# Performance work log

Hardware: AMD Instinct MI355X
Metric: run time of the kernel (lower is better)

Reference implementation:

```python
import jax, jax.numpy as jnp
import numpy as np

# config (matches init_kwargs)
NA, NEN = 8, 8            # n_agents, n_enemies
NENT = NA + NEN           # n_entities
NFA, NFE = 64, 64         # state_nf_al, state_nf_en
E, A, M, HE = 64, 64, 32, 64  # entity_embed, attn_embed, mixing_embed, hypernet_embed
TD, TE = 64, 64           # task_repre_dim, task_repre_embed_dim
BS, SL = 64, 512


def setup_inputs() -> dict:
    key = jax.random.key(0)
    ks = iter(jax.random.split(key, 32))
    def rn(shape, scale=0.05):
        return jax.random.normal(next(ks), shape, dtype=jnp.float32) * scale
    return {
        "agent_qs": rn((BS, SL, NA), 1.0),
        "states": rn((BS, SL, NA * NFA + NEN * NFE), 1.0),
        "task_repre_mu": rn((BS, SL, NA, TD), 1.0),
        "ally_w": rn((NFA, E)), "ally_b": rn((E,)),
        "enemy_w": rn((NFE, E)), "enemy_b": rn((E,)),
        "q_w": rn((E, A)), "q_b": rn((A,)),
        "k_w": rn((E, A)), "k_b": rn((A,)),
        "hw1_w1": rn((E + NFA + TE, HE)), "hw1_b1": rn((HE,)),
        "hw1_w2": rn((HE, M)), "hw1_b2": rn((M,)),
        "hwf_w1": rn((E + TE, HE)), "hwf_b1": rn((HE,)),
        "hwf_w2": rn((HE, M)), "hwf_b2": rn((M,)),
        "hb1_w": rn((E + TE, M)), "hb1_b": rn((M,)),
        "v_w1": rn((E + TE, M)), "v_b1": rn((M,)),
        "v_w2": rn((M, 1)), "v_b2": rn((1,)),
        "tre_w": rn((TD, TE)), "tre_b": rn((TE,)),
    }


def reference(agent_qs, states, task_repre_mu,
              ally_w, ally_b, enemy_w, enemy_b,
              q_w, q_b, k_w, k_b,
              hw1_w1, hw1_b1, hw1_w2, hw1_b2,
              hwf_w1, hwf_b1, hwf_w2, hwf_b2,
              hb1_w, hb1_b, v_w1, v_b1, v_w2, v_b2,
              tre_w, tre_b):
    bs, sl = agent_qs.shape[:2]
    # decompose_state (state_last_action=False, state_timestep_number=False)
    ally = states[..., : NA * NFA].reshape(bs, sl, NA, NFA)      # [bs,sl,NA,NFA]
    enemy = states[..., NA * NFA:].reshape(bs, sl, NEN, NFE)     # [bs,sl,NEN,NFE]
    ally_e = ally @ ally_w + ally_b                              # [bs,sl,NA,E]
    enemy_e = enemy @ enemy_w + enemy_b                          # [bs,sl,NEN,E]
    ent = jnp.concatenate([ally_e, enemy_e], axis=2)             # [bs,sl,NENT,E]
    q = ent @ q_w + q_b                                          # [bs,sl,NENT,A]
    k = ent @ k_w + k_b
    energy = jnp.einsum('bsqa,bska->bsqk', q, k)                 # [bs,sl,NENT,NENT]
    # torch: F.softmax(energy, dim=1) on [B,n_ent,n_ent] -> softmax over query axis
    attn = jax.nn.softmax(energy, axis=2)
    # attn_out = bmm(value[B,E,n], attn[B,n,n]).mean(-1)
    attn_out = jnp.einsum('bsne,bsnk->bse', ent, attn) / NENT    # [bs,sl,E]

    mean_mu = task_repre_mu.mean(axis=-2)                        # [bs,sl,TD]
    tre = task_repre_mu @ tre_w + tre_b                          # [bs,sl,NA,TE]
    mean_tre = mean_mu @ tre_w + tre_b                           # [bs,sl,TE]

    ent_mix = jnp.concatenate([
        jnp.broadcast_to(attn_out[:, :, None, :], (bs, sl, NA, E)),
        ally, tre], axis=-1)                                     # [bs,sl,NA,E+NFA+TE]
    mix = jnp.concatenate([attn_out, mean_tre], axis=-1)         # [bs,sl,E+TE]

    w1 = jnp.abs(jax.nn.relu(ent_mix @ hw1_w1 + hw1_b1) @ hw1_w2 + hw1_b2)  # [bs,sl,NA,M]
    b1 = mix @ hb1_w + hb1_b                                     # [bs,sl,M]
    hidden = jax.nn.elu(jnp.einsum('bsn,bsnm->bsm', agent_qs, w1) + b1)     # [bs,sl,M]
    wf = jnp.abs(jax.nn.relu(mix @ hwf_w1 + hwf_b1) @ hwf_w2 + hwf_b2)      # [bs,sl,M]
    v = jax.nn.relu(mix @ v_w1 + v_b1) @ v_w2 + v_b2             # [bs,sl,1]
    q_tot = jnp.einsum('bsm,bsm->bs', hidden, wf)[..., None] + v # [bs,sl,1]
    return q_tot
```

## Files before the change

### kernel.cpp

```cpp
#include <hip/hip_runtime.h>
#include <math.h>


#define TOKS 32768

typedef __attribute__((ext_vector_type(8))) short short8;
typedef __attribute__((ext_vector_type(4))) float f32x4;

#define MFMA(a, b, c) __builtin_amdgcn_mfma_f32_16x16x32_bf16((a), (b), (c), 0, 0, 0)

#define E_CAT   0
#define E_WQKT  8192
#define E_ZBRT  13312
#define E_H1T   29696
#define E_W2T   41984
#define E_WFT   44032
#define E_BF16_TOTAL 46080
#define E_AO_US 46464

__device__ __forceinline__ unsigned short bfr(float x) {
    unsigned u = __builtin_bit_cast(unsigned, x);
    u += 0x7fffu + ((u >> 16) & 1u);
    return (unsigned short)(u >> 16);
}
__device__ __forceinline__ float bf2f(unsigned short h) {
    unsigned u = ((unsigned)h) << 16;
    return __builtin_bit_cast(float, u);
}
__device__ __forceinline__ short8 cvt8v(float4 a, float4 b) {
    short8 r;
    r[0] = (short)bfr(a.x); r[1] = (short)bfr(a.y);
    r[2] = (short)bfr(a.z); r[3] = (short)bfr(a.w);
    r[4] = (short)bfr(b.x); r[5] = (short)bfr(b.y);
    r[6] = (short)bfr(b.z); r[7] = (short)bfr(b.w);
    return r;
}
#define SWZ64(r, c)  ((((r) * 64)  + (c)) ^ (((r) & 7) << 3))
#define SWZ128(r, c) ((((r) * 128) + (c)) ^ (((r) & 7) << 3))
#define SWZ192(r, c) ((((r) * 192) + (c)) ^ (((r) & 7) << 3))

__global__ __launch_bounds__(256) void qmix_setup(
    const float* __restrict__ ally_w, const float* __restrict__ enemy_w,
    const float* __restrict__ q_w, const float* __restrict__ k_w,
    const float* __restrict__ k_b,
    const float* __restrict__ hw1_w1, const float* __restrict__ hw1_b1,
    const float* __restrict__ hw1_w2,
    const float* __restrict__ hwf_w1, const float* __restrict__ hwf_b1,
    const float* __restrict__ hwf_w2,
    const float* __restrict__ hb1_w, const float* __restrict__ hb1_b,
    const float* __restrict__ v_w1, const float* __restrict__ v_b1,
    const float* __restrict__ tre_w, const float* __restrict__ tre_b,
    unsigned short* __restrict__ wsb, float* __restrict__ wsf)
{
    int gid = blockIdx.x * 256 + threadIdx.x;
    if (gid < E_BF16_TOTAL) {
        float v = 0.f;
        int base, r, c, K;
        if (gid < E_WQKT) {
            base = E_CAT; K = 128;
            int i = gid - base; r = i >> 7; c = i & 127;
            v = (c < 64) ? ally_w[c * 64 + r] : enemy_w[(c - 64) * 64 + r];
        } else if (gid < E_ZBRT) {
            base = E_WQKT; K = 64;
            int i = gid - base; r = i >> 6; c = i & 63;
            if (r < 64) {
                for (int g = 0; g < 64; ++g) v += q_w[c * 64 + g] * k_w[r * 64 + g];
            } else if (r == 64) {
                for (int g = 0; g < 64; ++g) v += q_w[c * 64 + g] * k_b[g];
            }
        } else if (gid < E_H1T) {
            base = E_ZBRT; K = 128;
            int i = gid - base; r = i >> 7; c = i & 127;
            if (r < 64) {
                if (c < 64) v = hwf_w1[c * 64 + r];
                else for (int g = 0; g < 64; ++g) v += tre_w[(c - 64) * 64 + g] * hwf_w1[(64 + g) * 64 + r];
            } else if (r < 96) {
                int m = r - 64;
                if (c < 64) v = hb1_w[c * 32 + m];
                else for (int g = 0; g < 64; ++g) v += tre_w[(c - 64) * 64 + g] * hb1_w[(64 + g) * 32 + m];
            } else {
                int m = r - 96;
                if (c < 64) v = v_w1[c * 32 + m];
                else for (int g = 0; g < 64; ++g) v += tre_w[(c - 64) * 64 + g] * v_w1[(64 + g) * 32 + m];
            }
        } else if (gid < E_W2T) {
            base = E_H1T; K = 192;
            int i = gid - base; r = i / 192; c = i % 192;
            if (c < 64) v = hw1_w1[(64 + c) * 64 + r];
            else if (c < 128) {
                for (int g = 0; g < 64; ++g) v += tre_w[(c - 64) * 64 + g] * hw1_w1[(128 + g) * 64 + r];
            } else v = hw1_w1[(c - 128) * 64 + r];
        } else if (gid < E_WFT) {
            base = E_W2T; K = 64;
            int i = gid - base; r = i >> 6; c = i & 63;
            v = hw1_w2[c * 32 + r];
        } else {
            base = E_WFT; K = 64;
            int i = gid - base; r = i >> 6; c = i & 63;
            v = hwf_w2[c * 32 + r];
        }
        wsb[base + ((r * K + c) ^ ((r & 7) << 3))] = bfr(v);
    } else if (gid < E_BF16_TOTAL + 192) {
        int j = gid - E_BF16_TOTAL; float v;
        if (j < 64) {
            v = hw1_b1[j];
            for (int g = 0; g < 64; ++g) v += tre_b[g] * hw1_w1[(128 + g) * 64 + j];
        } else if (j < 128) {
            int e = j - 64; v = hwf_b1[e];
            for (int g = 0; g < 64; ++g) v += tre_b[g] * hwf_w1[(64 + g) * 64 + e];
        } else if (j < 160) {
            int m = j - 128; v = hb1_b[m];
            for (int g = 0; g < 64; ++g) v += tre_b[g] * hb1_w[(64 + g) * 32 + m];
        } else {
            int m = j - 160; v = v_b1[m];
            for (int g = 0; g < 64; ++g) v += tre_b[g] * v_w1[(64 + g) * 32 + m];
        }
        wsf[j] = v;
    }
}

__global__ __launch_bounds__(512) void qmix_attn(
    const float* __restrict__ states,
    const float* __restrict__ ally_b, const float* __restrict__ enemy_b,
    const unsigned short* __restrict__ wsb,
    unsigned short* __restrict__ aoG)
{
    __shared__ unsigned short sWa[13312];
    __shared__ unsigned short sE[8][1024];
    __shared__ unsigned short sT[8][1024];

    const int lane = threadIdx.x & 63;
    const int wv   = threadIdx.x >> 6;
    const int l15  = lane & 15;
    const int lg   = lane >> 4;
    const int kb   = lg * 8;
    const size_t t = (size_t)blockIdx.x * 8 + wv;

    const short8 zero8 = {0, 0, 0, 0, 0, 0, 0, 0};
    const f32x4  zero4 = {0.f, 0.f, 0.f, 0.f};

    for (int i = threadIdx.x * 8; i < 13312; i += 512 * 8)
        *(short8*)(sWa + i) = *(const short8*)(wsb + E_CAT + i);

    const int roff = (l15 < 8) ? (l15 * 64 + kb) : (512 + (l15 - 8) * 64 + kb);
    const float* p = states + t * 1024 + roff;
    float4 cur0 = *(const float4*)(p);
    float4 cur1 = *(const float4*)(p + 4);
    float4 cur2 = *(const float4*)(p + 32);
    float4 cur3 = *(const float4*)(p + 36);

    float biasEnt[4];
    #pragma unroll
    for (int nt = 0; nt < 4; ++nt) {
        int col = nt * 16 + l15;
        biasEnt[nt] = (lg < 2) ? ally_b[col] : enemy_b[col];
    }
    __syncthreads();
    const unsigned short* lCAT  = sWa;
    const unsigned short* lWQKT = sWa + 8192;

    unsigned short* E = sE[wv];
    unsigned short* T = sT[wv];

    short8 a01 = cvt8v(cur0, cur1);
    short8 a23 = cvt8v(cur2, cur3);
    const bool isally = (l15 < 8);

    f32x4 accB[4] = {zero4, zero4, zero4, zero4};
    #pragma unroll
    for (int ks = 0; ks < 4; ++ks) {
        short8 af;
        if (ks == 0)      af = isally ? a01 : zero8;
        else if (ks == 1) af = isally ? a23 : zero8;
        else if (ks == 2) af = isally ? zero8 : a01;
        else              af = isally ? zero8 : a23;
        #pragma unroll
        for (int nt = 0; nt < 4; ++nt) {
            short8 w = *(const short8*)&lCAT[SWZ128(nt * 16 + l15, ks * 32 + kb)];
            accB[nt] = MFMA(af, w, accB[nt]);
        }
    }
    float entv[4][4];
    #pragma unroll
    for (int nt = 0; nt < 4; ++nt) {
        #pragma unroll
        for (int reg = 0; reg < 4; ++reg) {
            entv[nt][reg] = accB[nt][reg] + biasEnt[nt];
            E[SWZ64(lg * 4 + reg, nt * 16 + l15)] = bfr(entv[nt][reg]);
        }
    }

    f32x4 accC[5] = {zero4, zero4, zero4, zero4, zero4};
    short8 ef0 = *(const short8*)&E[SWZ64(l15, 0 * 32 + kb)];
    short8 ef1 = *(const short8*)&E[SWZ64(l15, 1 * 32 + kb)];
    #pragma unroll
    for (int nt = 0; nt < 5; ++nt) {
        short8 w0 = *(const short8*)&lWQKT[SWZ64(nt * 16 + l15, 0 * 32 + kb)];
        short8 w1 = *(const short8*)&lWQKT[SWZ64(nt * 16 + l15, 1 * 32 + kb)];
        accC[nt] = MFMA(ef0, w0, accC[nt]);
        accC[nt] = MFMA(ef1, w1, accC[nt]);
    }
    const int src = lane & 48;
    float si[4];
    #pragma unroll
    for (int reg = 0; reg < 4; ++reg) si[reg] = __shfl(accC[4][reg], src);
    #pragma unroll
    for (int nt = 0; nt < 4; ++nt)
        #pragma unroll
        for (int reg = 0; reg < 4; ++reg)
            T[SWZ64(lg * 4 + reg, nt * 16 + l15)] = bfr(accC[nt][reg]);

    f32x4 en = zero4;
    {
        short8 ta0 = *(const short8*)&T[SWZ64(l15, 0 * 32 + kb)];
        short8 ta1 = *(const short8*)&T[SWZ64(l15, 1 * 32 + kb)];
        en = MFMA(ta0, ef0, en);
        en = MFMA(ta1, ef1, en);
    }
    #pragma unroll
    for (int reg = 0; reg < 4; ++reg) en[reg] += si[reg];

    float mx = fmaxf(fmaxf(en[0], en[1]), fmaxf(en[2], en[3]));
    mx = fmaxf(mx, __shfl_xor(mx, 16));
    mx = fmaxf(mx, __shfl_xor(mx, 32));
    float p0 = __expf(en[0] - mx), p1 = __expf(en[1] - mx);
    float p2 = __expf(en[2] - mx), p3 = __expf(en[3] - mx);
    float s = p0 + p1 + p2 + p3;
    s += __shfl_xor(s, 16);
    s += __shfl_xor(s, 32);
    float inv = 1.f / s;
    float r0 = p0 * inv, r1 = p1 * inv, r2 = p2 * inv, r3 = p3 * inv;
    r0 += __shfl_xor(r0, 1); r0 += __shfl_xor(r0, 2); r0 += __shfl_xor(r0, 4); r0 += __shfl_xor(r0, 8);
    r1 += __shfl_xor(r1, 1); r1 += __shfl_xor(r1, 2); r1 += __shfl_xor(r1, 4); r1 += __shfl_xor(r1, 8);
    r2 += __shfl_xor(r2, 1); r2 += __shfl_xor(r2, 2); r2 += __shfl_xor(r2, 4); r2 += __shfl_xor(r2, 8);
    r3 += __shfl_xor(r3, 1); r3 += __shfl_xor(r3, 2); r3 += __shfl_xor(r3, 4); r3 += __shfl_xor(r3, 8);

    float part[4];
    #pragma unroll
    for (int nt = 0; nt < 4; ++nt) {
        float pp = r0 * entv[nt][0] + r1 * entv[nt][1]
                 + r2 * entv[nt][2] + r3 * entv[nt][3];
        pp += __shfl_xor(pp, 16);
        pp += __shfl_xor(pp, 32);
        part[nt] = pp;
    }
    float ao = (lg == 0) ? part[0] : (lg == 1) ? part[1]
             : (lg == 2) ? part[2] : part[3];
    aoG[t * 64 + lane] = bfr(ao * 0.0625f);
}

__global__ __launch_bounds__(512) void qmix_hyper(
    const float* __restrict__ agent_qs, const float* __restrict__ states,
    const float* __restrict__ mu,
    const float* __restrict__ v_w2, const float* __restrict__ v_b2,
    const float* __restrict__ hw1_b2, const float* __restrict__ hwf_b2,
    const unsigned short* __restrict__ wsb, const float* __restrict__ wsf,
    const unsigned short* __restrict__ aoG,
    float* __restrict__ out)
{
    __shared__ unsigned short sWb[16384];
    __shared__ unsigned short sMM[8192];
    __shared__ unsigned short sZT[8][1024];
    __shared__ float sB1[8][256];
    __shared__ float sWF[8][256];
    __shared__ float sV[8][8];

    const int tid  = threadIdx.x;
    const int lane = tid & 63;
    const int wv   = tid >> 6;
    const int l15  = lane & 15;
    const int lg   = lane >> 4;
    const int kb   = lg * 8;
    const int T0   = blockIdx.x * 64 + wv * 8;
    const int tokB = blockIdx.x * 64;

    const float* BH1 = wsf + 0;
    const float* BHF = wsf + 64;
    const float* BB1 = wsf + 128;
    const float* BV  = wsf + 160;

    const short8 zero8 = {0, 0, 0, 0, 0, 0, 0, 0};
    const f32x4  zero4 = {0.f, 0.f, 0.f, 0.f};

    for (int i = tid * 8; i < 16384; i += 512 * 8)
        *(short8*)(sWb + i) = *(const short8*)(wsb + E_ZBRT + i);

    {
        const size_t row = (size_t)(T0 + (l15 & 7));
    }
    short8 zA0 = *(const short8*)&aoG[(size_t)(T0 + (l15 & 7)) * 64 + kb];
    short8 zA1 = *(const short8*)&aoG[(size_t)(T0 + (l15 & 7)) * 64 + 32 + kb];

    {
        int tok = tid >> 3;
        int e8  = (tid & 7) * 8;
        const float* mp = mu + (size_t)(tokB + tok) * 512 + e8;
        float s0 = 0.f, s1 = 0.f, s2 = 0.f, s3 = 0.f,
              s4 = 0.f, s5 = 0.f, s6 = 0.f, s7 = 0.f;
        #pragma unroll
        for (int a = 0; a < 8; ++a) {
            float4 u = *(const float4*)(mp + a * 64);
            float4 v = *(const float4*)(mp + a * 64 + 4);
            s0 += u.x; s1 += u.y; s2 += u.z; s3 += u.w;
            s4 += v.x; s5 += v.y; s6 += v.z; s7 += v.w;
        }
        short8 r;
        r[0] = (short)bfr(s0 * 0.125f); r[1] = (short)bfr(s1 * 0.125f);
        r[2] = (short)bfr(s2 * 0.125f); r[3] = (short)bfr(s3 * 0.125f);
        r[4] = (short)bfr(s4 * 0.125f); r[5] = (short)bfr(s5 * 0.125f);
        r[6] = (short)bfr(s6 * 0.125f); r[7] = (short)bfr(s7 * 0.125f);
        *(short8*)&sMM[SWZ64(tok, e8)] = r;
    }
    for (int i = lane; i < 512; i += 64) sZT[wv][512 + i] = 0;
    __syncthreads();

    f32x4 zb[8] = {zero4, zero4, zero4, zero4, zero4, zero4, zero4, zero4};
    const bool arow = (l15 < 8);
    #pragma unroll
    for (int ks = 0; ks < 4; ++ks) {
        short8 af;
        if (ks == 0)      af = arow ? zA0 : zero8;
        else if (ks == 1) af = arow ? zA1 : zero8;
        else {
            short8 m = *(const short8*)&sMM[SWZ64(wv * 8 + (l15 & 7), (ks - 2) * 32 + kb)];
            af = arow ? m : zero8;
        }
        #pragma unroll
        for (int nt = 0; nt < 8; ++nt) {
            short8 w = *(const short8*)&sWb[SWZ128(nt * 16 + l15, ks * 32 + kb)];
            zb[nt] = MFMA(af, w, zb[nt]);
        }
    }
    __syncthreads();

    for (int i = tid * 8; i < 16384; i += 512 * 8)
        *(short8*)(sWb + i) = *(const short8*)(wsb + E_H1T + i);

    if (lg < 2) {
        #pragma unroll
        for (int nt = 0; nt < 4; ++nt) {
            int col = nt * 16 + l15;
            float bz = BHF[col];
            #pragma unroll
            for (int reg = 0; reg < 4; ++reg)
                sZT[wv][SWZ64(lg * 4 + reg, col)] = bfr(fmaxf(zb[nt][reg] + bz, 0.f));
        }
        #pragma unroll
        for (int nt = 4; nt < 6; ++nt) {
            int m = (nt - 4) * 16 + l15;
            float bb = BB1[m];
            #pragma unroll
            for (int reg = 0; reg < 4; ++reg)
                sB1[wv][(lg * 4 + reg) * 32 + m] = zb[nt][reg] + bb;
        }
    }
    {
        float bv0 = BV[l15], bv1 = BV[16 + l15];
        float vw0 = v_w2[l15], vw1 = v_w2[16 + l15];
        #pragma unroll
        for (int reg = 0; reg < 4; ++reg) {
            float vp = fmaxf(zb[6][reg] + bv0, 0.f) * vw0
                     + fmaxf(zb[7][reg] + bv1, 0.f) * vw1;
            vp += __shfl_xor(vp, 1); vp += __shfl_xor(vp, 2);
            vp += __shfl_xor(vp, 4); vp += __shfl_xor(vp, 8);
            if (l15 == 0 && lg < 2) sV[wv][lg * 4 + reg] = vp;
        }
    }
    __syncthreads();
    const unsigned short* lH1T = sWb;
    const unsigned short* lW2T = sWb + 12288;
    const unsigned short* lWFT = sWb + 14336;

    {
        f32x4 wfa = zero4, wfb = zero4;
        #pragma unroll
        for (int ks = 0; ks < 2; ++ks) {
            short8 af = *(const short8*)&sZT[wv][SWZ64(l15, ks * 32 + kb)];
            short8 b0 = *(const short8*)&lWFT[SWZ64(l15, ks * 32 + kb)];
            short8 b1 = *(const short8*)&lWFT[SWZ64(16 + l15, ks * 32 + kb)];
            wfa = MFMA(af, b0, wfa);
            wfb = MFMA(af, b1, wfb);
        }
        if (lg < 2) {
            float hb0 = hwf_b2[l15], hb1 = hwf_b2[16 + l15];
            #pragma unroll
            for (int reg = 0; reg < 4; ++reg) {
                int tok = lg * 4 + reg;
                sWF[wv][tok * 32 + l15]      = fabsf(wfa[reg] + hb0);
                sWF[wv][tok * 32 + 16 + l15] = fabsf(wfb[reg] + hb1);
            }
        }
    }

    const float vb2 = v_b2[0];
    const float b20 = hw1_b2[l15], b21 = hw1_b2[16 + l15];
    const int agent = l15 & 7;
    const int toff  = l15 >> 3;
    unsigned short* tile = sZT[wv];

    float4 cs0, cs1, cs2, cs3, cm0, cm1, cm2, cm3;
    short8 ca0, ca1;
    {
        const size_t tokA = (size_t)(T0 + toff);
        const float* sp = states + tokA * 1024 + agent * 64 + kb;
        const float* mp = mu + tokA * 512 + agent * 64 + kb;
        cs0 = *(const float4*)sp;        cs1 = *(const float4*)(sp + 4);
        cs2 = *(const float4*)(sp + 32); cs3 = *(const float4*)(sp + 36);
        cm0 = *(const float4*)mp;        cm1 = *(const float4*)(mp + 4);
        cm2 = *(const float4*)(mp + 32); cm3 = *(const float4*)(mp + 36);
        ca0 = *(const short8*)&aoG[tokA * 64 + kb];
        ca1 = *(const short8*)&aoG[tokA * 64 + 32 + kb];
    }

    for (int mc = 0; mc < 4; ++mc) {
        float4 us0 = cs0, us1 = cs1, us2 = cs2, us3 = cs3;
        float4 um0 = cm0, um1 = cm1, um2 = cm2, um3 = cm3;
        short8 ua0 = ca0, ua1 = ca1;
        if (mc < 3) {
            const size_t tokA = (size_t)(T0 + (mc + 1) * 2 + toff);
            const float* sp = states + tokA * 1024 + agent * 64 + kb;
            const float* mp = mu + tokA * 512 + agent * 64 + kb;
            cs0 = *(const float4*)sp;        cs1 = *(const float4*)(sp + 4);
            cs2 = *(const float4*)(sp + 32); cs3 = *(const float4*)(sp + 36);
            cm0 = *(const float4*)mp;        cm1 = *(const float4*)(mp + 4);
            cm2 = *(const float4*)(mp + 32); cm3 = *(const float4*)(mp + 36);
            ca0 = *(const short8*)&aoG[tokA * 64 + kb];
            ca1 = *(const short8*)&aoG[tokA * 64 + 32 + kb];
        }
        short8 f0 = cvt8v(us0, us1), f1 = cvt8v(us2, us3);
        short8 f2 = cvt8v(um0, um1), f3 = cvt8v(um2, um3);

        f32x4 h[4] = {zero4, zero4, zero4, zero4};
        #pragma unroll
        for (int ks = 0; ks < 6; ++ks) {
            short8 af = (ks == 0) ? f0 : (ks == 1) ? f1 : (ks == 2) ? f2
                      : (ks == 3) ? f3 : (ks == 4) ? ua0 : ua1;
            #pragma unroll
            for (int nt = 0; nt < 4; ++nt) {
                short8 w = *(const short8*)&lH1T[SWZ192(nt * 16 + l15, ks * 32 + kb)];
                h[nt] = MFMA(af, w, h[nt]);
            }
        }
        #pragma unroll
        for (int nt = 0; nt < 4; ++nt) {
            int col = nt * 16 + l15;
            float bh = BH1[col];
            #pragma unroll
            for (int reg = 0; reg < 4; ++reg)
                tile[SWZ64(lg * 4 + reg, col)] = bfr(fmaxf(h[nt][reg] + bh, 0.f));
        }

        f32x4 wa = zero4, wb = zero4;
        #pragma unroll
        for (int ks = 0; ks < 2; ++ks) {
            short8 af = *(const short8*)&tile[SWZ64(l15, ks * 32 + kb)];
            short8 b0 = *(const short8*)&lW2T[SWZ64(l15, ks * 32 + kb)];
            short8 b1 = *(const short8*)&lW2T[SWZ64(16 + l15, ks * 32 + kb)];
            wa = MFMA(af, b0, wa);
            wb = MFMA(af, b1, wb);
        }

        float hp0 = 0.f, hp1 = 0.f;
        #pragma unroll
        for (int reg = 0; reg < 4; ++reg) {
            int row = lg * 4 + reg;
            float qsv = agent_qs[(size_t)(T0 + mc * 2 + (row >> 3)) * 8 + (row & 7)];
            hp0 += qsv * fabsf(wa[reg] + b20);
            hp1 += qsv * fabsf(wb[reg] + b21);
        }
        hp0 += __shfl_xor(hp0, 16);
        hp1 += __shfl_xor(hp1, 16);
        int tokL = mc * 2 + (lg >> 1);
        float e0 = hp0 + sB1[wv][tokL * 32 + l15];
        float e1 = hp1 + sB1[wv][tokL * 32 + 16 + l15];
        float hid0 = e0 > 0.f ? e0 : (__expf(e0) - 1.f);
        float hid1 = e1 > 0.f ? e1 : (__expf(e1) - 1.f);
        float q = hid0 * sWF[wv][tokL * 32 + l15]
                + hid1 * sWF[wv][tokL * 32 + 16 + l15];
        q += __shfl_xor(q, 1); q += __shfl_xor(q, 2);
        q += __shfl_xor(q, 4); q += __shfl_xor(q, 8);
        if (l15 == 0 && (lg & 1) == 0)
            out[T0 + tokL] = q + sV[wv][tokL] + vb2;
    }
}

extern "C" void kernel_launch(void* const* d_in, const int* in_sizes, int n_in,
                              void* d_out, int out_size, void* d_ws, size_t ws_size,
                              hipStream_t stream)
{
    const float* agent_qs = (const float*)d_in[0];
    const float* states   = (const float*)d_in[1];
    const float* mu       = (const float*)d_in[2];
    const float* ally_w   = (const float*)d_in[3];
    const float* ally_b   = (const float*)d_in[4];
    const float* enemy_w  = (const float*)d_in[5];
    const float* enemy_b  = (const float*)d_in[6];
    const float* q_w      = (const float*)d_in[7];
    const float* k_w      = (const float*)d_in[9];
    const float* k_b      = (const float*)d_in[10];
    const float* hw1_w1   = (const float*)d_in[11];
    const float* hw1_b1   = (const float*)d_in[12];
    const float* hw1_w2   = (const float*)d_in[13];
    const float* hw1_b2   = (const float*)d_in[14];
    const float* hwf_w1   = (const float*)d_in[15];
    const float* hwf_b1   = (const float*)d_in[16];
    const float* hwf_w2   = (const float*)d_in[17];
    const float* hwf_b2   = (const float*)d_in[18];
    const float* hb1_w    = (const float*)d_in[19];
    const float* hb1_b    = (const float*)d_in[20];
    const float* v_w1     = (const float*)d_in[21];
    const float* v_b1     = (const float*)d_in[22];
    const float* v_w2     = (const float*)d_in[23];
    const float* v_b2     = (const float*)d_in[24];
    const float* tre_w    = (const float*)d_in[25];
    const float* tre_b    = (const float*)d_in[26];

    unsigned short* wsb = (unsigned short*)d_ws;
    float* wsf = (float*)((char*)d_ws + (size_t)E_BF16_TOTAL * 2);
    unsigned short* aoG = wsb + E_AO_US;
    float* out = (float*)d_out;

    hipLaunchKernelGGL(qmix_setup, dim3(181), dim3(256), 0, stream,
                       ally_w, enemy_w, q_w, k_w, k_b,
                       hw1_w1, hw1_b1, hw1_w2,
                       hwf_w1, hwf_b1, hwf_w2,
                       hb1_w, hb1_b, v_w1, v_b1, tre_w, tre_b,
                       wsb, wsf);

    hipLaunchKernelGGL(qmix_attn, dim3(TOKS / 8), dim3(512), 0, stream,
                       states, ally_b, enemy_b, wsb, aoG);

    hipLaunchKernelGGL(qmix_hyper, dim3(TOKS / 64), dim3(512), 0, stream,
                       agent_qs, states, mu, v_w2, v_b2, hw1_b2, hwf_b2,
                       wsb, wsf, aoG, out);
}
```

Measured before the change: 88.72 us.

## Fuse attention and hypernet kernels into one per-64-token kernel

Merges the attention kernel into the hypernetwork kernel so each wave computes attention outputs for its 8 tokens in a loop and keeps them in shared memory, removing the global round trip of attention outputs and one kernel launch. Shared memory is reorganized and reused (weights buffer shared across stages, b1 and wf stored as bf16 in per-wave tiles), and the task-mean computation moves into registers per lane. The trade-off is far fewer blocks for the attention phase (512 instead of 4096), so less parallelism and latency hiding for that stage, plus slight extra bf16 rounding of b1 and wf.

```diff
diff --git a/kernel.cpp b/kernel.cpp
--- a/kernel.cpp
+++ b/kernel.cpp
@@ -16,7 +16,6 @@
 #define E_W2T   41984
 #define E_WFT   44032
 #define E_BF16_TOTAL 46080
-#define E_AO_US 46464
 
 __device__ __forceinline__ unsigned short bfr(float x) {
     unsigned u = __builtin_bit_cast(unsigned, x);
@@ -119,150 +118,32 @@
     }
 }
 
-__global__ __launch_bounds__(512) void qmix_attn(
-    const float* __restrict__ states,
-    const float* __restrict__ ally_b, const float* __restrict__ enemy_b,
-    const unsigned short* __restrict__ wsb,
-    unsigned short* __restrict__ aoG)
-{
-    __shared__ unsigned short sWa[13312];
-    __shared__ unsigned short sE[8][1024];
-    __shared__ unsigned short sT[8][1024];
-
-    const int lane = threadIdx.x & 63;
-    const int wv   = threadIdx.x >> 6;
-    const int l15  = lane & 15;
-    const int lg   = lane >> 4;
-    const int kb   = lg * 8;
-    const size_t t = (size_t)blockIdx.x * 8 + wv;
-
-    const short8 zero8 = {0, 0, 0, 0, 0, 0, 0, 0};
-    const f32x4  zero4 = {0.f, 0.f, 0.f, 0.f};
-
-    for (int i = threadIdx.x * 8; i < 13312; i += 512 * 8)
-        *(short8*)(sWa + i) = *(const short8*)(wsb + E_CAT + i);
-
-    const int roff = (l15 < 8) ? (l15 * 64 + kb) : (512 + (l15 - 8) * 64 + kb);
-    const float* p = states + t * 1024 + roff;
-    float4 cur0 = *(const float4*)(p);
-    float4 cur1 = *(const float4*)(p + 4);
-    float4 cur2 = *(const float4*)(p + 32);
-    float4 cur3 = *(const float4*)(p + 36);
-
-    float biasEnt[4];
+__device__ __forceinline__ short8 mmfrag(const float* __restrict__ mp) {
+    float a0 = 0.f, a1 = 0.f, a2 = 0.f, a3 = 0.f, a4 = 0.f, a5 = 0.f, a6 = 0.f, a7 = 0.f;
     #pragma unroll
-    for (int nt = 0; nt < 4; ++nt) {
-        int col = nt * 16 + l15;
-        biasEnt[nt] = (lg < 2) ? ally_b[col] : enemy_b[col];
-    }
-    __syncthreads();
-    const unsigned short* lCAT  = sWa;
-    const unsigned short* lWQKT = sWa + 8192;
-
-    unsigned short* E = sE[wv];
-    unsigned short* T = sT[wv];
-
-    short8 a01 = cvt8v(cur0, cur1);
-    short8 a23 = cvt8v(cur2, cur3);
-    const bool isally = (l15 < 8);
-
-    f32x4 accB[4] = {zero4, zero4, zero4, zero4};
-    #pragma unroll
-    for (int ks = 0; ks < 4; ++ks) {
-        short8 af;
-        if (ks == 0)      af = isally ? a01 : zero8;
-        else if (ks == 1) af = isally ? a23 : zero8;
-        else if (ks == 2) af = isally ? zero8 : a01;
-        else              af = isally ? zero8 : a23;
-        #pragma unroll
-        for (int nt = 0; nt < 4; ++nt) {
-            short8 w = *(const short8*)&lCAT[SWZ128(nt * 16 + l15, ks * 32 + kb)];
-            accB[nt] = MFMA(af, w, accB[nt]);
-        }
-    }
-    float entv[4][4];
-    #pragma unroll
-    for (int nt = 0; nt < 4; ++nt) {
-        #pragma unroll
-        for (int reg = 0; reg < 4; ++reg) {
-            entv[nt][reg] = accB[nt][reg] + biasEnt[nt];
-            E[SWZ64(lg * 4 + reg, nt * 16 + l15)] = bfr(entv[nt][reg]);
-        }
-    }
-
-    f32x4 accC[5] = {zero4, zero4, zero4, zero4, zero4};
-    short8 ef0 = *(const short8*)&E[SWZ64(l15, 0 * 32 + kb)];
-    short8 ef1 = *(const short8*)&E[SWZ64(l15, 1 * 32 + kb)];
-    #pragma unroll
-    for (int nt = 0; nt < 5; ++nt) {
-        short8 w0 = *(const short8*)&lWQKT[SWZ64(nt * 16 + l15, 0 * 32 + kb)];
-        short8 w1 = *(const short8*)&lWQKT[SWZ64(nt * 16 + l15, 1 * 32 + kb)];
-        accC[nt] = MFMA(ef0, w0, accC[nt]);
-        accC[nt] = MFMA(ef1, w1, accC[nt]);
-    }
-    const int src = lane & 48;
-    float si[4];
-    #pragma unroll
-    for (int reg = 0; reg < 4; ++reg) si[reg] = __shfl(accC[4][reg], src);
-    #pragma unroll
-    for (int nt = 0; nt < 4; ++nt)
-        #pragma unroll
-        for (int reg = 0; reg < 4; ++reg)
-            T[SWZ64(lg * 4 + reg, nt * 16 + l15)] = bfr(accC[nt][reg]);
-
-    f32x4 en = zero4;
-    {
-        short8 ta0 = *(const short8*)&T[SWZ64(l15, 0 * 32 + kb)];
-        short8 ta1 = *(const short8*)&T[SWZ64(l15, 1 * 32 + kb)];
-        en = MFMA(ta0, ef0, en);
-        en = MFMA(ta1, ef1, en);
-    }
-    #pragma unroll
-    for (int reg = 0; reg < 4; ++reg) en[reg] += si[reg];
-
-    float mx = fmaxf(fmaxf(en[0], en[1]), fmaxf(en[2], en[3]));
-    mx = fmaxf(mx, __shfl_xor(mx, 16));
-    mx = fmaxf(mx, __shfl_xor(mx, 32));
-    float p0 = __expf(en[0] - mx), p1 = __expf(en[1] - mx);
-    float p2 = __expf(en[2] - mx), p3 = __expf(en[3] - mx);
-    float s = p0 + p1 + p2 + p3;
-    s += __shfl_xor(s, 16);
-    s += __shfl_xor(s, 32);
-    float inv = 1.f / s;
-    float r0 = p0 * inv, r1 = p1 * inv, r2 = p2 * inv, r3 = p3 * inv;
-    r0 += __shfl_xor(r0, 1); r0 += __shfl_xor(r0, 2); r0 += __shfl_xor(r0, 4); r0 += __shfl_xor(r0, 8);
-    r1 += __shfl_xor(r1, 1); r1 += __shfl_xor(r1, 2); r1 += __shfl_xor(r1, 4); r1 += __shfl_xor(r1, 8);
-    r2 += __shfl_xor(r2, 1); r2 += __shfl_xor(r2, 2); r2 += __shfl_xor(r2, 4); r2 += __shfl_xor(r2, 8);
-    r3 += __shfl_xor(r3, 1); r3 += __shfl_xor(r3, 2); r3 += __shfl_xor(r3, 4); r3 += __shfl_xor(r3, 8);
-
-    float part[4];
-    #pragma unroll
-    for (int nt = 0; nt < 4; ++nt) {
-        float pp = r0 * entv[nt][0] + r1 * entv[nt][1]
-                 + r2 * entv[nt][2] + r3 * entv[nt][3];
-        pp += __shfl_xor(pp, 16);
-        pp += __shfl_xor(pp, 32);
-        part[nt] = pp;
-    }
-    float ao = (lg == 0) ? part[0] : (lg == 1) ? part[1]
-             : (lg == 2) ? part[2] : part[3];
-    aoG[t * 64 + lane] = bfr(ao * 0.0625f);
-}
-
-__global__ __launch_bounds__(512) void qmix_hyper(
+    for (int a = 0; a < 8; ++a) {
+        float4 u = *(const float4*)(mp + a * 64);
+        float4 v = *(const float4*)(mp + a * 64 + 4);
+        a0 += u.x; a1 += u.y; a2 += u.z; a3 += u.w;
+        a4 += v.x; a5 += v.y; a6 += v.z; a7 += v.w;
+    }
+    return cvt8v(make_float4(a0 * 0.125f, a1 * 0.125f, a2 * 0.125f, a3 * 0.125f),
+                 make_float4(a4 * 0.125f, a5 * 0.125f, a6 * 0.125f, a7 * 0.125f));
+}
+
+__global__ __launch_bounds__(512) void qmix_fused(
     const float* __restrict__ agent_qs, const float* __restrict__ states,
     const float* __restrict__ mu,
+    const float* __restrict__ ally_b, const float* __restrict__ enemy_b,
     const float* __restrict__ v_w2, const float* __restrict__ v_b2,
     const float* __restrict__ hw1_b2, const float* __restrict__ hwf_b2,
     const unsigned short* __restrict__ wsb, const float* __restrict__ wsf,
-    const unsigned short* __restrict__ aoG,
     float* __restrict__ out)
 {
-    __shared__ unsigned short sWb[16384];
-    __shared__ unsigned short sMM[8192];
-    __shared__ unsigned short sZT[8][1024];
-    __shared__ float sB1[8][256];
-    __shared__ float sWF[8][256];
+    __shared__ unsigned short sW[16384];
+    __shared__ unsigned short sE[8][1024];
+    __shared__ unsigned short sT[8][1024];
+    __shared__ unsigned short sAO[8][512];
     __shared__ float sV[8][8];
 
     const int tid  = threadIdx.x;
@@ -272,7 +153,6 @@
     const int lg   = lane >> 4;
     const int kb   = lg * 8;
     const int T0   = blockIdx.x * 64 + wv * 8;
-    const int tokB = blockIdx.x * 64;
 
     const float* BH1 = wsf + 0;
     const float* BHF = wsf + 64;
@@ -282,36 +162,134 @@
     const short8 zero8 = {0, 0, 0, 0, 0, 0, 0, 0};
     const f32x4  zero4 = {0.f, 0.f, 0.f, 0.f};
 
+    unsigned short* E  = sE[wv];
+    unsigned short* T  = sT[wv];
+    unsigned short* AO = sAO[wv];
+
+    for (int i = tid * 8; i < 13312; i += 512 * 8)
+        *(short8*)(sW + i) = *(const short8*)(wsb + E_CAT + i);
+
+    float biasEnt[4];
+    #pragma unroll
+    for (int nt = 0; nt < 4; ++nt) {
+        int col = nt * 16 + l15;
+        biasEnt[nt] = (lg < 2) ? ally_b[col] : enemy_b[col];
+    }
+    const int roff = (l15 < 8) ? (l15 * 64 + kb) : (512 + (l15 - 8) * 64 + kb);
+    float4 pf[4];
+    {
+        const float* p = states + (size_t)T0 * 1024 + roff;
+        pf[0] = *(const float4*)(p);      pf[1] = *(const float4*)(p + 4);
+        pf[2] = *(const float4*)(p + 32); pf[3] = *(const float4*)(p + 36);
+    }
+    __syncthreads();
+    const unsigned short* lCAT  = sW;
+    const unsigned short* lWQKT = sW + 8192;
+
+    for (int ti = 0; ti < 8; ++ti) {
+        const size_t t = (size_t)(T0 + ti);
+        float4 cur0 = pf[0], cur1 = pf[1], cur2 = pf[2], cur3 = pf[3];
+        if (ti < 7) {
+            const float* p = states + (t + 1) * 1024 + roff;
+            pf[0] = *(const float4*)(p);      pf[1] = *(const float4*)(p + 4);
+            pf[2] = *(const float4*)(p + 32); pf[3] = *(const float4*)(p + 36);
+        }
+        short8 a01 = cvt8v(cur0, cur1);
+        short8 a23 = cvt8v(cur2, cur3);
+        const bool isally = (l15 < 8);
+
+        f32x4 accB[4] = {zero4, zero4, zero4, zero4};
+        #pragma unroll
+        for (int ks = 0; ks < 4; ++ks) {
+            short8 af;
+            if (ks == 0)      af = isally ? a01 : zero8;
+            else if (ks == 1) af = isally ? a23 : zero8;
+            else if (ks == 2) af = isally ? zero8 : a01;
+            else              af = isally ? zero8 : a23;
+            #pragma unroll
+            for (int nt = 0; nt < 4; ++nt) {
+                short8 w = *(const short8*)&lCAT[SWZ128(nt * 16 + l15, ks * 32 + kb)];
+                accB[nt] = MFMA(af, w, accB[nt]);
+            }
+        }
+        float entv[4][4];
+        #pragma unroll
+        for (int nt = 0; nt < 4; ++nt) {
+            #pragma unroll
+            for (int reg = 0; reg < 4; ++reg) {
+                entv[nt][reg] = accB[nt][reg] + biasEnt[nt];
+                E[SWZ64(lg * 4 + reg, nt * 16 + l15)] = bfr(entv[nt][reg]);
+            }
+        }
+
+        f32x4 accC[5] = {zero4, zero4, zero4, zero4, zero4};
+        short8 ef0 = *(const short8*)&E[SWZ64(l15, 0 * 32 + kb)];
+        short8 ef1 = *(const short8*)&E[SWZ64(l15, 1 * 32 + kb)];
+        #pragma unroll
+        for (int nt = 0; nt < 5; ++nt) {
+            short8 w0 = *(const short8*)&lWQKT[SWZ64(nt * 16 + l15, 0 * 32 + kb)];
+            short8 w1 = *(const short8*)&lWQKT[SWZ64(nt * 16 + l15, 1 * 32 + kb)];
+            accC[nt] = MFMA(ef0, w0, accC[nt]);
+            accC[nt] = MFMA(ef1, w1, accC[nt]);
+        }
+        const int src = lane & 48;
+        float si[4];
+        #pragma unroll
+        for (int reg = 0; reg < 4; ++reg) si[reg] = __shfl(accC[4][reg], src);
+        #pragma unroll
+        for (int nt = 0; nt < 4; ++nt)
+            #pragma unroll
+            for (int reg = 0; reg < 4; ++reg)
+                T[SWZ64(lg * 4 + reg, nt * 16 + l15)] = bfr(accC[nt][reg]);
+
+        f32x4 en = zero4;
+        {
+            short8 ta0 = *(const short8*)&T[SWZ64(l15, 0 * 32 + kb)];
+            short8 ta1 = *(const short8*)&T[SWZ64(l15, 1 * 32 + kb)];
+            en = MFMA(ta0, ef0, en);
+            en = MFMA(ta1, ef1, en);
+        }
+        #pragma unroll
+        for (int reg = 0; reg < 4; ++reg) en[reg] += si[reg];
+
+        float mx = fmaxf(fmaxf(en[0], en[1]), fmaxf(en[2], en[3]));
+        mx = fmaxf(mx, __shfl_xor(mx, 16));
+        mx = fmaxf(mx, __shfl_xor(mx, 32));
+        float p0 = __expf(en[0] - mx), p1 = __expf(en[1] - mx);
+        float p2 = __expf(en[2] - mx), p3 = __expf(en[3] - mx);
+        float s = p0 + p1 + p2 + p3;
+        s += __shfl_xor(s, 16);
+        s += __shfl_xor(s, 32);
+        float inv = 1.f / s;
+        float r0 = p0 * inv, r1 = p1 * inv, r2 = p2 * inv, r3 = p3 * inv;
+        r0 += __shfl_xor(r0, 1); r0 += __shfl_xor(r0, 2); r0 += __shfl_xor(r0, 4); r0 += __shfl_xor(r0, 8);
+        r1 += __shfl_xor(r1, 1); r1 += __shfl_xor(r1, 2); r1 += __shfl_xor(r1, 4); r1 += __shfl_xor(r1, 8);
+        r2 += __shfl_xor(r2, 1); r2 += __shfl_xor(r2, 2); r2 += __shfl_xor(r2, 4); r2 += __shfl_xor(r2, 8);
+        r3 += __shfl_xor(r3, 1); r3 += __shfl_xor(r3, 2); r3 += __shfl_xor(r3, 4); r3 += __shfl_xor(r3, 8);
+
+        float part[4];
+        #pragma unroll
+        for (int nt = 0; nt < 4; ++nt) {
+            float pp = r0 * entv[nt][0] + r1 * entv[nt][1]
+                     + r2 * entv[nt][2] + r3 * entv[nt][3];
+            pp += __shfl_xor(pp, 16);
+            pp += __shfl_xor(pp, 32);
+            part[nt] = pp;
+        }
+        float ao = (lg == 0) ? part[0] : (lg == 1) ? part[1]
+                 : (lg == 2) ? part[2] : part[3];
+        AO[SWZ64(ti, lane)] = bfr(ao * 0.0625f);
+    }
+    __syncthreads();
+
     for (int i = tid * 8; i < 16384; i += 512 * 8)
-        *(short8*)(sWb + i) = *(const short8*)(wsb + E_ZBRT + i);
-
-    {
-        const size_t row = (size_t)(T0 + (l15 & 7));
-    }
-    short8 zA0 = *(const short8*)&aoG[(size_t)(T0 + (l15 & 7)) * 64 + kb];
-    short8 zA1 = *(const short8*)&aoG[(size_t)(T0 + (l15 & 7)) * 64 + 32 + kb];
-
-    {
-        int tok = tid >> 3;
-        int e8  = (tid & 7) * 8;
-        const float* mp = mu + (size_t)(tokB + tok) * 512 + e8;
-        float s0 = 0.f, s1 = 0.f, s2 = 0.f, s3 = 0.f,
-              s4 = 0.f, s5 = 0.f, s6 = 0.f, s7 = 0.f;
-        #pragma unroll
-        for (int a = 0; a < 8; ++a) {
-            float4 u = *(const float4*)(mp + a * 64);
-            float4 v = *(const float4*)(mp + a * 64 + 4);
-            s0 += u.x; s1 += u.y; s2 += u.z; s3 += u.w;
-            s4 += v.x; s5 += v.y; s6 += v.z; s7 += v.w;
-        }
-        short8 r;
-        r[0] = (short)bfr(s0 * 0.125f); r[1] = (short)bfr(s1 * 0.125f);
-        r[2] = (short)bfr(s2 * 0.125f); r[3] = (short)bfr(s3 * 0.125f);
-        r[4] = (short)bfr(s4 * 0.125f); r[5] = (short)bfr(s5 * 0.125f);
-        r[6] = (short)bfr(s6 * 0.125f); r[7] = (short)bfr(s7 * 0.125f);
-        *(short8*)&sMM[SWZ64(tok, e8)] = r;
-    }
-    for (int i = lane; i < 512; i += 64) sZT[wv][512 + i] = 0;
+        *(short8*)(sW + i) = *(const short8*)(wsb + E_ZBRT + i);
+
+    const int arow8 = l15 & 7;
+    short8 mm2 = mmfrag(mu + (size_t)(T0 + arow8) * 512 + kb);
+    short8 mm3 = mmfrag(mu + (size_t)(T0 + arow8) * 512 + 32 + kb);
+    short8 zA0 = *(const short8*)&AO[SWZ64(arow8, kb)];
+    short8 zA1 = *(const short8*)&AO[SWZ64(arow8, 32 + kb)];
     __syncthreads();
 
     f32x4 zb[8] = {zero4, zero4, zero4, zero4, zero4, zero4, zero4, zero4};
@@ -321,21 +299,22 @@
         short8 af;
         if (ks == 0)      af = arow ? zA0 : zero8;
         else if (ks == 1) af = arow ? zA1 : zero8;
-        else {
-            short8 m = *(const short8*)&sMM[SWZ64(wv * 8 + (l15 & 7), (ks - 2) * 32 + kb)];
-            af = arow ? m : zero8;
-        }
+        else if (ks == 2) af = arow ? mm2 : zero8;
+        else              af = arow ? mm3 : zero8;
         #pragma unroll
         for (int nt = 0; nt < 8; ++nt) {
-            short8 w = *(const short8*)&sWb[SWZ128(nt * 16 + l15, ks * 32 + kb)];
+            short8 w = *(const short8*)&sW[SWZ128(nt * 16 + l15, ks * 32 + kb)];
             zb[nt] = MFMA(af, w, zb[nt]);
         }
     }
     __syncthreads();
 
     for (int i = tid * 8; i < 16384; i += 512 * 8)
-        *(short8*)(sWb + i) = *(const short8*)(wsb + E_H1T + i);
-
+        *(short8*)(sW + i) = *(const short8*)(wsb + E_H1T + i);
+
+    unsigned short* b1T = T + 512;
+    unsigned short* wfT = T + 768;
+    for (int i = lane; i < 512; i += 64) E[512 + i] = 0;
     if (lg < 2) {
         #pragma unroll
         for (int nt = 0; nt < 4; ++nt) {
@@ -343,7 +322,7 @@
             float bz = BHF[col];
             #pragma unroll
             for (int reg = 0; reg < 4; ++reg)
-                sZT[wv][SWZ64(lg * 4 + reg, col)] = bfr(fmaxf(zb[nt][reg] + bz, 0.f));
+                E[SWZ64(lg * 4 + reg, col)] = bfr(fmaxf(zb[nt][reg] + bz, 0.f));
         }
         #pragma unroll
         for (int nt = 4; nt < 6; ++nt) {
@@ -351,7 +330,7 @@
             float bb = BB1[m];
             #pragma unroll
             for (int reg = 0; reg < 4; ++reg)
-                sB1[wv][(lg * 4 + reg) * 32 + m] = zb[nt][reg] + bb;
+                b1T[(lg * 4 + reg) * 32 + m] = bfr(zb[nt][reg] + bb);
         }
     }
     {
@@ -366,40 +345,9 @@
             if (l15 == 0 && lg < 2) sV[wv][lg * 4 + reg] = vp;
         }
     }
-    __syncthreads();
-    const unsigned short* lH1T = sWb;
-    const unsigned short* lW2T = sWb + 12288;
-    const unsigned short* lWFT = sWb + 14336;
-
-    {
-        f32x4 wfa = zero4, wfb = zero4;
-        #pragma unroll
-        for (int ks = 0; ks < 2; ++ks) {
-            short8 af = *(const short8*)&sZT[wv][SWZ64(l15, ks * 32 + kb)];
-            short8 b0 = *(const short8*)&lWFT[SWZ64(l15, ks * 32 + kb)];
-            short8 b1 = *(const short8*)&lWFT[SWZ64(16 + l15, ks * 32 + kb)];
-            wfa = MFMA(af, b0, wfa);
-            wfb = MFMA(af, b1, wfb);
-        }
-        if (lg < 2) {
-            float hb0 = hwf_b2[l15], hb1 = hwf_b2[16 + l15];
-            #pragma unroll
-            for (int reg = 0; reg < 4; ++reg) {
-                int tok = lg * 4 + reg;
-                sWF[wv][tok * 32 + l15]      = fabsf(wfa[reg] + hb0);
-                sWF[wv][tok * 32 + 16 + l15] = fabsf(wfb[reg] + hb1);
-            }
-        }
-    }
-
-    const float vb2 = v_b2[0];
-    const float b20 = hw1_b2[l15], b21 = hw1_b2[16 + l15];
     const int agent = l15 & 7;
     const int toff  = l15 >> 3;
-    unsigned short* tile = sZT[wv];
-
     float4 cs0, cs1, cs2, cs3, cm0, cm1, cm2, cm3;
-    short8 ca0, ca1;
     {
         const size_t tokA = (size_t)(T0 + toff);
         const float* sp = states + tokA * 1024 + agent * 64 + kb;
@@ -408,14 +356,39 @@
         cs2 = *(const float4*)(sp + 32); cs3 = *(const float4*)(sp + 36);
         cm0 = *(const float4*)mp;        cm1 = *(const float4*)(mp + 4);
         cm2 = *(const float4*)(mp + 32); cm3 = *(const float4*)(mp + 36);
-        ca0 = *(const short8*)&aoG[tokA * 64 + kb];
-        ca1 = *(const short8*)&aoG[tokA * 64 + 32 + kb];
-    }
+    }
+    __syncthreads();
+    const unsigned short* lH1T = sW;
+    const unsigned short* lW2T = sW + 12288;
+    const unsigned short* lWFT = sW + 14336;
+
+    {
+        f32x4 wfa = zero4, wfb = zero4;
+        #pragma unroll
+        for (int ks = 0; ks < 2; ++ks) {
+            short8 af = *(const short8*)&E[SWZ64(l15, ks * 32 + kb)];
+            short8 b0 = *(const short8*)&lWFT[SWZ64(l15, ks * 32 + kb)];
+            short8 b1 = *(const short8*)&lWFT[SWZ64(16 + l15, ks * 32 + kb)];
+            wfa = MFMA(af, b0, wfa);
+            wfb = MFMA(af, b1, wfb);
+        }
+        if (lg < 2) {
+            float hb0 = hwf_b2[l15], hb1 = hwf_b2[16 + l15];
+            #pragma unroll
+            for (int reg = 0; reg < 4; ++reg) {
+                int tok = lg * 4 + reg;
+                wfT[tok * 32 + l15]      = bfr(fabsf(wfa[reg] + hb0));
+                wfT[tok * 32 + 16 + l15] = bfr(fabsf(wfb[reg] + hb1));
+            }
+        }
+    }
+
+    const float vb2 = v_b2[0];
+    const float b20 = hw1_b2[l15], b21 = hw1_b2[16 + l15];
 
     for (int mc = 0; mc < 4; ++mc) {
         float4 us0 = cs0, us1 = cs1, us2 = cs2, us3 = cs3;
         float4 um0 = cm0, um1 = cm1, um2 = cm2, um3 = cm3;
-        short8 ua0 = ca0, ua1 = ca1;
         if (mc < 3) {
             const size_t tokA = (size_t)(T0 + (mc + 1) * 2 + toff);
             const float* sp = states + tokA * 1024 + agent * 64 + kb;
@@ -424,11 +397,11 @@
             cs2 = *(const float4*)(sp + 32); cs3 = *(const float4*)(sp + 36);
             cm0 = *(const float4*)mp;        cm1 = *(const float4*)(mp + 4);
             cm2 = *(const float4*)(mp + 32); cm3 = *(const float4*)(mp + 36);
-            ca0 = *(const short8*)&aoG[tokA * 64 + kb];
-            ca1 = *(const short8*)&aoG[tokA * 64 + 32 + kb];
         }
         short8 f0 = cvt8v(us0, us1), f1 = cvt8v(us2, us3);
         short8 f2 = cvt8v(um0, um1), f3 = cvt8v(um2, um3);
+        short8 ua0 = *(const short8*)&AO[SWZ64(mc * 2 + toff, kb)];
+        short8 ua1 = *(const short8*)&AO[SWZ64(mc * 2 + toff, 32 + kb)];
 
         f32x4 h[4] = {zero4, zero4, zero4, zero4};
         #pragma unroll
@@ -447,13 +420,13 @@
             float bh = BH1[col];
             #pragma unroll
             for (int reg = 0; reg < 4; ++reg)
-                tile[SWZ64(lg * 4 + reg, col)] = bfr(fmaxf(h[nt][reg] + bh, 0.f));
+                E[SWZ64(lg * 4 + reg, col)] = bfr(fmaxf(h[nt][reg] + bh, 0.f));
         }
 
         f32x4 wa = zero4, wb = zero4;
         #pragma unroll
         for (int ks = 0; ks < 2; ++ks) {
-            short8 af = *(const short8*)&tile[SWZ64(l15, ks * 32 + kb)];
+            short8 af = *(const short8*)&E[SWZ64(l15, ks * 32 + kb)];
             short8 b0 = *(const short8*)&lW2T[SWZ64(l15, ks * 32 + kb)];
             short8 b1 = *(const short8*)&lW2T[SWZ64(16 + l15, ks * 32 + kb)];
             wa = MFMA(af, b0, wa);
@@ -471,12 +444,12 @@
         hp0 += __shfl_xor(hp0, 16);
         hp1 += __shfl_xor(hp1, 16);
         int tokL = mc * 2 + (lg >> 1);
-        float e0 = hp0 + sB1[wv][tokL * 32 + l15];
-        float e1 = hp1 + sB1[wv][tokL * 32 + 16 + l15];
+        float e0 = hp0 + bf2f(b1T[tokL * 32 + l15]);
+        float e1 = hp1 + bf2f(b1T[tokL * 32 + 16 + l15]);
         float hid0 = e0 > 0.f ? e0 : (__expf(e0) - 1.f);
         float hid1 = e1 > 0.f ? e1 : (__expf(e1) - 1.f);
-        float q = hid0 * sWF[wv][tokL * 32 + l15]
-                + hid1 * sWF[wv][tokL * 32 + 16 + l15];
+        float q = hid0 * bf2f(wfT[tokL * 32 + l15])
+                + hid1 * bf2f(wfT[tokL * 32 + 16 + l15]);
         q += __shfl_xor(q, 1); q += __shfl_xor(q, 2);
         q += __shfl_xor(q, 4); q += __shfl_xor(q, 8);
         if (l15 == 0 && (lg & 1) == 0)
@@ -517,7 +490,6 @@
 
     unsigned short* wsb = (unsigned short*)d_ws;
     float* wsf = (float*)((char*)d_ws + (size_t)E_BF16_TOTAL * 2);
-    unsigned short* aoG = wsb + E_AO_US;
     float* out = (float*)d_out;
 
     hipLaunchKernelGGL(qmix_setup, dim3(181), dim3(256), 0, stream,
@@ -527,10 +499,8 @@
                        hb1_w, hb1_b, v_w1, v_b1, tre_w, tre_b,
                        wsb, wsf);
 
-    hipLaunchKernelGGL(qmix_attn, dim3(TOKS / 8), dim3(512), 0, stream,
-                       states, ally_b, enemy_b, wsb, aoG);
-
-    hipLaunchKernelGGL(qmix_hyper, dim3(TOKS / 64), dim3(512), 0, stream,
-                       agent_qs, states, mu, v_w2, v_b2, hw1_b2, hwf_b2,
-                       wsb, wsf, aoG, out);
-}
+    hipLaunchKernelGGL(qmix_fused, dim3(TOKS / 64), dim3(512), 0, stream,
+                       agent_qs, states, mu, ally_b, enemy_b,
+                       v_w2, v_b2, hw1_b2, hwf_b2,
+                       wsb, wsf, out);
+}
```

After: 98.40 us. +10.9%, slower.
